# Performance work log

Hardware: AMD Instinct MI355X
Metric: run time of the kernel (lower is better)

Reference implementation:

```python
import jax, jax.numpy as jnp
import numpy as np

B, L, D, H, K = 32, 2048, 512, 256, 4  # batch, bag_size, input_dim, hidden_dim, n_attentions


def setup_inputs() -> dict:
    key = jax.random.key(0)
    k_x, k1, k1b, k2, k2b, k3, k3b = jax.random.split(key, 7)
    s1 = 1.0 / np.sqrt(D)
    s2 = 1.0 / np.sqrt(H)
    return {
        "x": jax.random.normal(k_x, (B * L, D), dtype=jnp.float32),
        "W1": jax.random.uniform(k1, (D, H), jnp.float32, -s1, s1),
        "b1": jax.random.uniform(k1b, (H,), jnp.float32, -s1, s1),
        "W3": jax.random.uniform(k3, (D, H), jnp.float32, -s1, s1),
        "b3": jax.random.uniform(k3b, (H,), jnp.float32, -s1, s1),
        "W2": jax.random.uniform(k2, (H, K), jnp.float32, -s2, s2),
        "b2": jax.random.uniform(k2b, (K,), jnp.float32, -s2, s2),
        "bag_lengths": jnp.full((B,), L, dtype=jnp.int32),
    }


def reference(x, W1, b1, W3, b3, W2, b2, bag_lengths):
    batch = bag_lengths.shape[0]
    bag = x.shape[0] // batch  # equal-length bags (fast path in original)
    # gated attention MLP, per instance: [N, K]
    A = jnp.tanh(x @ W1 + b1) * jax.nn.sigmoid(x @ W3 + b3)
    A = A @ W2 + b2
    # per-bag softmax over instances, per attention head
    A = A.reshape(batch, bag, K).transpose(0, 2, 1)  # [B, K, L]
    A = jax.nn.softmax(A, axis=2)
    # attention-weighted sum of instances -> [B, K, D] -> [B, K*D]
    out = jnp.einsum('bkl,bld->bkd', A, x.reshape(batch, bag, -1))
    return out.reshape(batch, -1)
```

## Files before the change

kernel.cpp:

```cpp
#include <hip/hip_runtime.h>
#include <hip/hip_bf16.h>


typedef short  bf16x8 __attribute__((ext_vector_type(8)));
typedef float  f32x4  __attribute__((ext_vector_type(4)));

#define D_IN    512
#define H_DIM   256
#define L_BAG   2048

__device__ __forceinline__ short f2bf(float f) {
  union { float f; unsigned u; } u;
  u.f = f;
  unsigned r = u.u + 0x7FFFu + ((u.u >> 16) & 1u);
  return (short)(r >> 16);
}
__device__ __forceinline__ float bf2f(short s) {
  union { float f; unsigned u; } u;
  u.u = ((unsigned)(unsigned short)s) << 16;
  return u.f;
}

__global__ __launch_bounds__(256) void k_prep_w(const float* __restrict__ W1,
                                                const float* __restrict__ W3,
                                                short* __restrict__ wc) {
  int t = blockIdx.x * 256 + threadIdx.x;
  int n_c = t & 511;
  int kc  = t >> 9;
  int kt = kc >> 2, c = kc & 3;
  int g = n_c >> 5, j = n_c & 31;
  const float* src = (j < 16) ? W1 : W3;
  int h = g * 16 + (j & 15);
  bf16x8 v;
  #pragma unroll
  for (int r = 0; r < 8; ++r) v[r] = f2bf(src[(kc * 8 + r) * H_DIM + h]);
  *(bf16x8*)(wc + kt * 16384 + (c * 512 + n_c) * 8) = v;
}

__global__ __launch_bounds__(512, 4) void k_fused(
    const float* __restrict__ x,
    const short* __restrict__ wc,
    const float* __restrict__ b1, const float* __restrict__ b3,
    const float* __restrict__ W2,
    short* __restrict__ part, float* __restrict__ psumP)
{
  __shared__ __align__(16) short xbf[64 * 512];
  __shared__ float lpart[8][64][4];
  __shared__ __align__(16) float wlds[64 * 4];
  __shared__ float psc[4][4];

  const int tid  = threadIdx.x;
  const int lane = tid & 63;
  const int w    = tid >> 6;
  const int l15  = lane & 15;
  const int q    = lane >> 4;
  const int blk  = blockIdx.x;
  const long row0 = (long)blk * 64;

  {
    const int r   = tid & 63;
    const int kc0 = (tid >> 6) * 8;
    const float* xr = x + (row0 + r) * D_IN + kc0 * 8;
    #pragma unroll
    for (int j = 0; j < 8; ++j) {
      float4 f0 = ((const float4*)(xr + j * 8))[0];
      float4 f1 = ((const float4*)(xr + j * 8))[1];
      bf16x8 v;
      v[0] = f2bf(f0.x); v[1] = f2bf(f0.y); v[2] = f2bf(f0.z); v[3] = f2bf(f0.w);
      v[4] = f2bf(f1.x); v[5] = f2bf(f1.y); v[6] = f2bf(f1.z); v[7] = f2bf(f1.w);
      *(bf16x8*)&xbf[((kc0 + j) * 64 + r) * 8] = v;
    }
  }
  __syncthreads();

  f32x4 acc[4][4];
  #pragma unroll
  for (int mf = 0; mf < 4; ++mf)
    #pragma unroll
    for (int nf = 0; nf < 4; ++nf) acc[mf][nf] = (f32x4){0.f, 0.f, 0.f, 0.f};

  const short* bgp = wc + (q * 512 + w * 64 + l15) * 8;

  #pragma unroll 1
  for (int kt = 0; kt < 16; ++kt) {
    bf16x8 af[4], bfr[4];
    const short* bk = bgp + kt * 16384;
    #pragma unroll
    for (int nf = 0; nf < 4; ++nf)
      bfr[nf] = *(const bf16x8*)(bk + nf * 128);
    const int ab = (kt * 4 + q) * 512 + l15 * 8;
    #pragma unroll
    for (int mf = 0; mf < 4; ++mf)
      af[mf] = *(const bf16x8*)&xbf[ab + mf * 128];
    #pragma unroll
    for (int mf = 0; mf < 4; ++mf)
      #pragma unroll
      for (int nf = 0; nf < 4; ++nf)
        acc[mf][nf] = __builtin_amdgcn_mfma_f32_16x16x32_bf16(af[mf], bfr[nf], acc[mf][nf], 0, 0, 0);
  }

  float b1v[2], b3v[2];
  f32x4 wv[2];
  #pragma unroll
  for (int p = 0; p < 2; ++p) {
    int h = w * 32 + p * 16 + l15;
    b1v[p] = b1[h];
    b3v[p] = b3[h];
    wv[p] = *(const f32x4*)&W2[h * 4];
  }
  #pragma unroll
  for (int mf = 0; mf < 4; ++mf) {
    float pl[4][4];
    #pragma unroll
    for (int j = 0; j < 4; ++j)
      #pragma unroll
      for (int kk = 0; kk < 4; ++kk) pl[j][kk] = 0.f;
    #pragma unroll
    for (int p = 0; p < 2; ++p)
      #pragma unroll
      for (int j = 0; j < 4; ++j) {
        float h1 = acc[mf][2 * p][j]     + b1v[p];
        float h3 = acc[mf][2 * p + 1][j] + b3v[p];
        float A = __expf(2.f * h1);
        float B = __expf(-h3);
        float g = (A - 1.f) * __builtin_amdgcn_rcpf((A + 1.f) * (1.f + B));
        pl[j][0] += g * wv[p][0];
        pl[j][1] += g * wv[p][1];
        pl[j][2] += g * wv[p][2];
        pl[j][3] += g * wv[p][3];
      }
    #pragma unroll
    for (int off = 1; off < 16; off <<= 1)
      #pragma unroll
      for (int j = 0; j < 4; ++j)
        #pragma unroll
        for (int kk = 0; kk < 4; ++kk)
          pl[j][kk] += __shfl_xor(pl[j][kk], off);
    if (l15 == 0) {
      #pragma unroll
      for (int j = 0; j < 4; ++j)
        #pragma unroll
        for (int kk = 0; kk < 4; ++kk)
          lpart[w][mf * 16 + q * 4 + j][kk] = pl[j][kk];
    }
  }
  __syncthreads();

  if (tid < 256) {
    const int r = tid >> 2, kk = tid & 3;
    float lg = 0.f;
    #pragma unroll
    for (int ww = 0; ww < 8; ++ww) lg += lpart[ww][r][kk];
    float e = __expf(lg);
    wlds[r * 4 + kk] = e;
    float v = e;
    #pragma unroll
    for (int o = 4; o < 64; o <<= 1) v += __shfl_xor(v, o);
    if (lane < 4) psc[tid >> 6][lane] = v;
  }
  __syncthreads();
  if (tid < 4) psumP[blk * 4 + tid] = psc[0][tid] + psc[1][tid] + psc[2][tid] + psc[3][tid];

  {
    const int d  = tid;
    const int kc = d >> 3;
    const int e  = d & 7;
    const short* xcol = &xbf[kc * 512 + e];
    float a0 = 0.f, a1 = 0.f, a2 = 0.f, a3 = 0.f;
    #pragma unroll 8
    for (int ii = 0; ii < 64; ++ii) {
      int l = (ii + kc) & 63;
      float xf = bf2f(xcol[l * 8]);
      float4 wv4 = *(const float4*)&wlds[l * 4];
      a0 += wv4.x * xf; a1 += wv4.y * xf; a2 += wv4.z * xf; a3 += wv4.w * xf;
    }
    short* pp = part + (long)blk * 2048 + d;
    pp[0]    = f2bf(a0);
    pp[512]  = f2bf(a1);
    pp[1024] = f2bf(a2);
    pp[1536] = f2bf(a3);
  }
}

__global__ __launch_bounds__(256) void k_finalize(const short* __restrict__ part,
                                                  const float* __restrict__ psumP,
                                                  float* __restrict__ out) {
  int idx = blockIdx.x * 256 + threadIdx.x;
  int b = idx >> 11, k = (idx >> 9) & 3, d = idx & 511;
  const short* pb = part + ((long)b * 32) * 2048 + k * 512 + d;
  float s = 0.f, ps = 0.f;
  #pragma unroll
  for (int c = 0; c < 32; ++c) {
    s  += bf2f(pb[c * 2048]);
    ps += psumP[(b * 32 + c) * 4 + k];
  }
  out[idx] = s / ps;
}

extern "C" void kernel_launch(void* const* d_in, const int* in_sizes, int n_in,
                              void* d_out, int out_size, void* d_ws, size_t ws_size,
                              hipStream_t stream) {
  const float* x  = (const float*)d_in[0];
  const float* W1 = (const float*)d_in[1];
  const float* b1 = (const float*)d_in[2];
  const float* W3 = (const float*)d_in[3];
  const float* b3 = (const float*)d_in[4];
  const float* W2 = (const float*)d_in[5];
  float* out = (float*)d_out;

  char* ws = (char*)d_ws;
  short* wc    = (short*)(ws + 0);
  short* part  = (short*)(ws + 524288);
  float* psumP = (float*)(ws + 524288 + 4194304);

  hipLaunchKernelGGL(k_prep_w,   dim3(128),  dim3(256), 0, stream, W1, W3, wc);
  hipLaunchKernelGGL(k_fused,    dim3(1024), dim3(512), 0, stream, x, wc, b1, b3, W2, part, psumP);
  hipLaunchKernelGGL(k_finalize, dim3(256),  dim3(256), 0, stream, part, psumP, out);
}
```

Measured before the change: 78.73 us.

## Process 64-row tile as two 32-row halves to cut LDS and raise occupancy

The fused kernel now stages x for 32 rows at a time in LDS, looping twice per block and carrying the partial weighted sums and exp-sums across halves in shared memory. This roughly halves LDS and accumulator registers per block, and the launch bound now targets 6 blocks per CU instead of 4 so more waves can hide memory latency. In exchange, each block pays extra barriers and serial phases, and each MFMA pass reuses the weight fragments over fewer rows.

```diff
diff --git a/kernel.cpp b/kernel.cpp
--- a/kernel.cpp
+++ b/kernel.cpp
@@ -37,17 +37,19 @@
   *(bf16x8*)(wc + kt * 16384 + (c * 512 + n_c) * 8) = v;
 }
 
-__global__ __launch_bounds__(512, 4) void k_fused(
+__global__ __launch_bounds__(512, 6) void k_fused(
     const float* __restrict__ x,
     const short* __restrict__ wc,
     const float* __restrict__ b1, const float* __restrict__ b3,
     const float* __restrict__ W2,
     short* __restrict__ part, float* __restrict__ psumP)
 {
-  __shared__ __align__(16) short xbf[64 * 512];
-  __shared__ float lpart[8][64][4];
-  __shared__ __align__(16) float wlds[64 * 4];
-  __shared__ float psc[4][4];
+  __shared__ __align__(16) short xbf[32 * 512];
+  __shared__ float lpart[8][32][4];
+  __shared__ __align__(16) float wlds[32 * 4];
+  __shared__ __align__(16) float pacc[512 * 4];
+  __shared__ float psc[2][4];
+  __shared__ float psacc[4];
 
   const int tid  = threadIdx.x;
   const int lane = tid & 63;
@@ -55,130 +57,149 @@
   const int l15  = lane & 15;
   const int q    = lane >> 4;
   const int blk  = blockIdx.x;
-  const long row0 = (long)blk * 64;
-
-  {
-    const int r   = tid & 63;
-    const int kc0 = (tid >> 6) * 8;
-    const float* xr = x + (row0 + r) * D_IN + kc0 * 8;
+
+  const int sr   = tid & 31;
+  const int skc0 = (tid >> 5) * 4;
+
+  #pragma unroll 1
+  for (int t = 0; t < 2; ++t) {
+    const long row0 = (long)blk * 64 + t * 32;
+
+    {
+      const float* xr = x + (row0 + sr) * D_IN + skc0 * 8;
+      #pragma unroll
+      for (int j = 0; j < 4; ++j) {
+        float4 f0 = ((const float4*)(xr + j * 8))[0];
+        float4 f1 = ((const float4*)(xr + j * 8))[1];
+        bf16x8 v;
+        v[0] = f2bf(f0.x); v[1] = f2bf(f0.y); v[2] = f2bf(f0.z); v[3] = f2bf(f0.w);
+        v[4] = f2bf(f1.x); v[5] = f2bf(f1.y); v[6] = f2bf(f1.z); v[7] = f2bf(f1.w);
+        *(bf16x8*)&xbf[((skc0 + j) * 32 + sr) * 8] = v;
+      }
+    }
+    __syncthreads();
+
+    f32x4 acc[2][4];
     #pragma unroll
-    for (int j = 0; j < 8; ++j) {
-      float4 f0 = ((const float4*)(xr + j * 8))[0];
-      float4 f1 = ((const float4*)(xr + j * 8))[1];
-      bf16x8 v;
-      v[0] = f2bf(f0.x); v[1] = f2bf(f0.y); v[2] = f2bf(f0.z); v[3] = f2bf(f0.w);
-      v[4] = f2bf(f1.x); v[5] = f2bf(f1.y); v[6] = f2bf(f1.z); v[7] = f2bf(f1.w);
-      *(bf16x8*)&xbf[((kc0 + j) * 64 + r) * 8] = v;
-    }
-  }
-  __syncthreads();
-
-  f32x4 acc[4][4];
-  #pragma unroll
-  for (int mf = 0; mf < 4; ++mf)
-    #pragma unroll
-    for (int nf = 0; nf < 4; ++nf) acc[mf][nf] = (f32x4){0.f, 0.f, 0.f, 0.f};
-
-  const short* bgp = wc + (q * 512 + w * 64 + l15) * 8;
-
-  #pragma unroll 1
-  for (int kt = 0; kt < 16; ++kt) {
-    bf16x8 af[4], bfr[4];
-    const short* bk = bgp + kt * 16384;
-    #pragma unroll
-    for (int nf = 0; nf < 4; ++nf)
-      bfr[nf] = *(const bf16x8*)(bk + nf * 128);
-    const int ab = (kt * 4 + q) * 512 + l15 * 8;
-    #pragma unroll
-    for (int mf = 0; mf < 4; ++mf)
-      af[mf] = *(const bf16x8*)&xbf[ab + mf * 128];
-    #pragma unroll
-    for (int mf = 0; mf < 4; ++mf)
+    for (int mf = 0; mf < 2; ++mf)
+      #pragma unroll
+      for (int nf = 0; nf < 4; ++nf) acc[mf][nf] = (f32x4){0.f, 0.f, 0.f, 0.f};
+
+    const short* bgp = wc + (q * 512 + w * 64 + l15) * 8;
+
+    #pragma unroll 1
+    for (int kt = 0; kt < 16; ++kt) {
+      bf16x8 af[2], bfr[4];
+      const short* bk = bgp + kt * 16384;
       #pragma unroll
       for (int nf = 0; nf < 4; ++nf)
-        acc[mf][nf] = __builtin_amdgcn_mfma_f32_16x16x32_bf16(af[mf], bfr[nf], acc[mf][nf], 0, 0, 0);
-  }
-
-  float b1v[2], b3v[2];
-  f32x4 wv[2];
-  #pragma unroll
-  for (int p = 0; p < 2; ++p) {
-    int h = w * 32 + p * 16 + l15;
-    b1v[p] = b1[h];
-    b3v[p] = b3[h];
-    wv[p] = *(const f32x4*)&W2[h * 4];
-  }
-  #pragma unroll
-  for (int mf = 0; mf < 4; ++mf) {
-    float pl[4][4];
-    #pragma unroll
-    for (int j = 0; j < 4; ++j)
-      #pragma unroll
-      for (int kk = 0; kk < 4; ++kk) pl[j][kk] = 0.f;
-    #pragma unroll
-    for (int p = 0; p < 2; ++p)
-      #pragma unroll
-      for (int j = 0; j < 4; ++j) {
-        float h1 = acc[mf][2 * p][j]     + b1v[p];
-        float h3 = acc[mf][2 * p + 1][j] + b3v[p];
-        float A = __expf(2.f * h1);
-        float B = __expf(-h3);
-        float g = (A - 1.f) * __builtin_amdgcn_rcpf((A + 1.f) * (1.f + B));
-        pl[j][0] += g * wv[p][0];
-        pl[j][1] += g * wv[p][1];
-        pl[j][2] += g * wv[p][2];
-        pl[j][3] += g * wv[p][3];
-      }
-    #pragma unroll
-    for (int off = 1; off < 16; off <<= 1)
-      #pragma unroll
-      for (int j = 0; j < 4; ++j)
-        #pragma unroll
-        for (int kk = 0; kk < 4; ++kk)
-          pl[j][kk] += __shfl_xor(pl[j][kk], off);
-    if (l15 == 0) {
-      #pragma unroll
-      for (int j = 0; j < 4; ++j)
-        #pragma unroll
-        for (int kk = 0; kk < 4; ++kk)
-          lpart[w][mf * 16 + q * 4 + j][kk] = pl[j][kk];
-    }
-  }
-  __syncthreads();
-
-  if (tid < 256) {
-    const int r = tid >> 2, kk = tid & 3;
-    float lg = 0.f;
-    #pragma unroll
-    for (int ww = 0; ww < 8; ++ww) lg += lpart[ww][r][kk];
-    float e = __expf(lg);
-    wlds[r * 4 + kk] = e;
-    float v = e;
-    #pragma unroll
-    for (int o = 4; o < 64; o <<= 1) v += __shfl_xor(v, o);
-    if (lane < 4) psc[tid >> 6][lane] = v;
-  }
-  __syncthreads();
-  if (tid < 4) psumP[blk * 4 + tid] = psc[0][tid] + psc[1][tid] + psc[2][tid] + psc[3][tid];
-
-  {
-    const int d  = tid;
-    const int kc = d >> 3;
-    const int e  = d & 7;
-    const short* xcol = &xbf[kc * 512 + e];
-    float a0 = 0.f, a1 = 0.f, a2 = 0.f, a3 = 0.f;
-    #pragma unroll 8
-    for (int ii = 0; ii < 64; ++ii) {
-      int l = (ii + kc) & 63;
-      float xf = bf2f(xcol[l * 8]);
-      float4 wv4 = *(const float4*)&wlds[l * 4];
-      a0 += wv4.x * xf; a1 += wv4.y * xf; a2 += wv4.z * xf; a3 += wv4.w * xf;
-    }
-    short* pp = part + (long)blk * 2048 + d;
-    pp[0]    = f2bf(a0);
-    pp[512]  = f2bf(a1);
-    pp[1024] = f2bf(a2);
-    pp[1536] = f2bf(a3);
+        bfr[nf] = *(const bf16x8*)(bk + nf * 128);
+      const int ab = (kt * 4 + q) * 256 + l15 * 8;
+      #pragma unroll
+      for (int mf = 0; mf < 2; ++mf)
+        af[mf] = *(const bf16x8*)&xbf[ab + mf * 128];
+      #pragma unroll
+      for (int mf = 0; mf < 2; ++mf)
+        #pragma unroll
+        for (int nf = 0; nf < 4; ++nf)
+          acc[mf][nf] = __builtin_amdgcn_mfma_f32_16x16x32_bf16(af[mf], bfr[nf], acc[mf][nf], 0, 0, 0);
+    }
+
+    {
+      float b1v[2], b3v[2];
+      f32x4 wv[2];
+      #pragma unroll
+      for (int p = 0; p < 2; ++p) {
+        int h = w * 32 + p * 16 + l15;
+        b1v[p] = b1[h];
+        b3v[p] = b3[h];
+        wv[p] = *(const f32x4*)&W2[h * 4];
+      }
+      #pragma unroll
+      for (int mf = 0; mf < 2; ++mf) {
+        float pl[4][4];
+        #pragma unroll
+        for (int j = 0; j < 4; ++j)
+          #pragma unroll
+          for (int kk = 0; kk < 4; ++kk) pl[j][kk] = 0.f;
+        #pragma unroll
+        for (int p = 0; p < 2; ++p)
+          #pragma unroll
+          for (int j = 0; j < 4; ++j) {
+            float h1 = acc[mf][2 * p][j]     + b1v[p];
+            float h3 = acc[mf][2 * p + 1][j] + b3v[p];
+            float A = __expf(2.f * h1);
+            float B = __expf(-h3);
+            float g = (A - 1.f) * __builtin_amdgcn_rcpf((A + 1.f) * (1.f + B));
+            pl[j][0] += g * wv[p][0];
+            pl[j][1] += g * wv[p][1];
+            pl[j][2] += g * wv[p][2];
+            pl[j][3] += g * wv[p][3];
+          }
+        #pragma unroll
+        for (int off = 1; off < 16; off <<= 1)
+          #pragma unroll
+          for (int j = 0; j < 4; ++j)
+            #pragma unroll
+            for (int kk = 0; kk < 4; ++kk)
+              pl[j][kk] += __shfl_xor(pl[j][kk], off);
+        if (l15 == 0) {
+          #pragma unroll
+          for (int j = 0; j < 4; ++j)
+            #pragma unroll
+            for (int kk = 0; kk < 4; ++kk)
+              lpart[w][mf * 16 + q * 4 + j][kk] = pl[j][kk];
+        }
+      }
+    }
+    __syncthreads();
+
+    if (tid < 128) {
+      const int r = tid >> 2, kk = tid & 3;
+      float lg = 0.f;
+      #pragma unroll
+      for (int ww = 0; ww < 8; ++ww) lg += lpart[ww][r][kk];
+      float e = __expf(lg);
+      wlds[r * 4 + kk] = e;
+      float v = e;
+      #pragma unroll
+      for (int o = 4; o < 64; o <<= 1) v += __shfl_xor(v, o);
+      if (lane < 4) psc[tid >> 6][lane] = v;
+    }
+    __syncthreads();
+
+    if (tid < 4) {
+      float s = psc[0][tid] + psc[1][tid];
+      if (t == 0) psacc[tid] = s;
+      else        psumP[blk * 4 + tid] = psacc[tid] + s;
+    }
+
+    {
+      const int d  = tid;
+      const int kc = d >> 3;
+      const int e  = d & 7;
+      const short* xcol = &xbf[kc * 256 + e];
+      float a0 = 0.f, a1 = 0.f, a2 = 0.f, a3 = 0.f;
+      #pragma unroll 8
+      for (int ii = 0; ii < 32; ++ii) {
+        int l = (ii + kc) & 31;
+        float xf = bf2f(xcol[l * 8]);
+        float4 wv4 = *(const float4*)&wlds[l * 4];
+        a0 += wv4.x * xf; a1 += wv4.y * xf; a2 += wv4.z * xf; a3 += wv4.w * xf;
+      }
+      if (t == 0) {
+        *(f32x4*)&pacc[d * 4] = (f32x4){a0, a1, a2, a3};
+      } else {
+        f32x4 prev = *(const f32x4*)&pacc[d * 4];
+        short* pp = part + (long)blk * 2048 + d;
+        pp[0]    = f2bf(prev[0] + a0);
+        pp[512]  = f2bf(prev[1] + a1);
+        pp[1024] = f2bf(prev[2] + a2);
+        pp[1536] = f2bf(prev[3] + a3);
+      }
+    }
+
+    if (t == 0) __syncthreads();
   }
 }
 
```

Result: slower. 96.43 us (+22.5%).
